# Performance work log

Measured on AMD Instinct MI355X. Metric: run time of the kernel, lower is better.

Reference implementation:

```python
import jax, jax.numpy as jnp
import numpy as np
import math

B, D, S, C, H = 8192, 512, 5, 2048, 4

def setup_inputs() -> dict:
    key = jax.random.key(0)
    ks = jax.random.split(key, 8)
    return {
        "features": jax.random.normal(ks[0], (B, D), dtype=jnp.float32),
        "logits": jax.random.normal(ks[1], (S, B, C), dtype=jnp.float32),
        "scale_feats": jax.random.normal(ks[2], (S, B, D), dtype=jnp.float32),
        "Wq": jax.random.normal(ks[3], (D, D), dtype=jnp.float32) * 0.02,
        "bq": jnp.zeros((D,), jnp.float32),
        "Wk": jax.random.normal(ks[4], (D, D), dtype=jnp.float32) * 0.02,
        "bk": jnp.zeros((D,), jnp.float32),
        "Wv": jax.random.normal(ks[5], (D, D), dtype=jnp.float32) * 0.02,
        "bv": jnp.zeros((D,), jnp.float32),
        "scale_emb": jax.random.normal(ks[6], (S, D), dtype=jnp.float32) * 0.02,
        "temperature": jnp.float32(0.07),
        "attn_w": jnp.ones((3,), jnp.float32) / 3.0,
    }

def reference(features, logits, scale_feats, Wq, bq, Wk, bk, Wv, bv, scale_emb, temperature, attn_w):
    b, d = features.shape
    s = scale_feats.shape[0]
    hd = d // H
    t = jnp.abs(temperature)

    # ---- multihead attention over scales (V is computed in torch but unused) ----
    Q = (features @ Wq + bq).reshape(b, H, hd)                      # [B,H,hd]
    sf_emb = scale_feats + scale_emb[:, None, :]                    # [S,B,D]
    K = (sf_emb @ Wk + bk).reshape(s, b, H, hd)                     # [S,B,H,hd]
    scores = jnp.einsum('bhd,sbhd->bhs', Q, K) / jnp.float32(math.sqrt(hd))
    attn_mha = jax.nn.softmax(scores / t, axis=-1).mean(axis=1)     # [B,S]

    # ---- geometric (angular) attention ----
    fn = features / jnp.linalg.norm(features, axis=-1, keepdims=True).clip(1e-12)
    sfn = scale_feats / jnp.linalg.norm(scale_feats, axis=-1, keepdims=True).clip(1e-12)
    cos_sim = jnp.einsum('bd,sbd->bs', fn, sfn)                     # [B,S]
    angles = jnp.arccos(jnp.clip(cos_sim, -1.0 + 1e-7, 1.0 - 1e-7))
    attn_geo = jax.nn.softmax(jnp.exp(-angles / t), axis=-1)        # [B,S]

    # ---- Cayley-Menger volume-proxy attention ----
    # simplex points: [features, scale_feat, cos(a)*f + sin(a)*s for a in {pi/4, pi/2, 3pi/4}]
    c = jnp.float32(math.sqrt(0.5))
    cf = jnp.array([1.0, 0.0, c, 0.0, -c], jnp.float32)             # coeffs on features
    cs = jnp.array([0.0, 1.0, c, 1.0, c], jnp.float32)              # coeffs on scale_feat
    simplex = (cf[None, :, None, None] * features[None, None] +
               cs[None, :, None, None] * scale_feats[:, None])      # [S,5,B,D]
    norms = jnp.sum(simplex * simplex, axis=-1)                     # [S,5,B]
    gram = jnp.einsum('spbd,sqbd->spqb', simplex, simplex)          # [S,5,5,B]
    distsq = norms[:, :, None] + norms[:, None, :] - 2.0 * gram     # [S,5,5,B]
    volumes = distsq.mean(axis=(1, 2)).T                            # [B,S]
    attn_cay = jax.nn.softmax(volumes / t, axis=-1)

    # ---- fuse attention types ----
    w = jax.nn.softmax(attn_w, axis=0)
    combined = w[0] * attn_mha + w[1] * attn_geo + w[2] * attn_cay  # [B,S]
    combined = combined / combined.sum(axis=-1, keepdims=True)

    combined_logits = jnp.einsum('bs,sbc->bc', combined, logits)    # [B,C]
    return (combined_logits, combined)
```

## Files before the change

### kernel.cpp

```cpp
#include <hip/hip_runtime.h>
#include <math.h>

#define B_N 8192
#define D_N 512
#define S_N 5
#define C_N 2048
#define H_N 4

typedef __attribute__((ext_vector_type(8))) short bf16x8;
typedef __attribute__((ext_vector_type(4))) float floatx4;

__device__ __forceinline__ float bf2f(short u) {
  union { unsigned int i; float f; } c;
  c.i = ((unsigned int)(unsigned short)u) << 16;
  return c.f;
}
__device__ __forceinline__ short f2bf(float f) {
  union { float f; unsigned int i; } c; c.f = f;
  unsigned int x = c.i;
  x += 0x7fffu + ((x >> 16) & 1u);
  return (short)(x >> 16);
}
__device__ __forceinline__ unsigned long long pack4(float a, float b, float c, float d) {
  return (unsigned long long)(unsigned short)f2bf(a)
       | ((unsigned long long)(unsigned short)f2bf(b) << 16)
       | ((unsigned long long)(unsigned short)f2bf(c) << 32)
       | ((unsigned long long)(unsigned short)f2bf(d) << 48);
}

__global__ __launch_bounds__(256) void k_prep(
    const float* __restrict__ f, const float* __restrict__ Wq,
    const float* __restrict__ Wk, short* __restrict__ fbf,
    short* __restrict__ WqT, short* __restrict__ Wkb) {
  __shared__ float lds[64][65];
  const int bx = blockIdx.x, t = threadIdx.x;
  if (bx < 2048) {
    int i = bx * 256 + t;
    const floatx4* p = (const floatx4*)(f + (size_t)i * 8);
    floatx4 a = p[0], b = p[1];
    *(unsigned long long*)(fbf + (size_t)i * 8)     = pack4(a[0], a[1], a[2], a[3]);
    *(unsigned long long*)(fbf + (size_t)i * 8 + 4) = pack4(b[0], b[1], b[2], b[3]);
  } else if (bx < 2112) {
    const int bb = bx - 2048;
    const int r0 = (bb >> 3) * 64, c0 = (bb & 7) * 64;
#pragma unroll
    for (int i = 0; i < 16; ++i) {
      int r = i * 4 + (t >> 6), c = t & 63;
      lds[r][c] = Wq[(size_t)(r0 + r) * 512 + c0 + c];
    }
    __syncthreads();
#pragma unroll
    for (int i = 0; i < 16; ++i) {
      int cL = i * 4 + (t >> 6), rL = t & 63;
      WqT[(size_t)(c0 + cL) * 512 + r0 + rL] = f2bf(lds[rL][cL]);
    }
  } else {
    const int base = (bx - 2112) * 8192 + t * 4;
#pragma unroll
    for (int i = 0; i < 8; ++i) {
      int idx = base + i * 1024;
      floatx4 v = *(const floatx4*)(Wk + idx);
      *(unsigned long long*)(Wkb + idx) = pack4(v[0], v[1], v[2], v[3]);
    }
  }
}

__device__ __forceinline__ void gll(const short* g, short* l) {
  __builtin_amdgcn_global_load_lds(
      (const __attribute__((address_space(1))) unsigned int*)(g),
      (__attribute__((address_space(3))) unsigned int*)(l), 16, 0, 0);
}

__global__ __launch_bounds__(256) void k_gemm64(
    const short* __restrict__ A, int lda,
    const short* __restrict__ BT, int ldb,
    short* __restrict__ O, int ldo,
    const float* __restrict__ bias, int K, int z_koff, int z_coff,
    float* __restrict__ qtp, const float* __restrict__ bkp) {
  __shared__ __align__(16) short As[2][2048];
  __shared__ __align__(16) short Bs[2][4096];
  __shared__ float qtLds[64][2];

  const int tid = threadIdx.x;
  const int lane = tid & 63;
  const int wid = tid >> 6;
  const int wr = wid >> 1, wc = wid & 1;
  const int row0 = blockIdx.y * 64;
  const int col0 = blockIdx.x * 128;
  const int z = blockIdx.z;
  const int koff = z * z_koff;
  const int ocoff = z * z_coff;

  const int r1 = tid >> 2, hk = tid & 3;
  const short* Ag1 = A + (size_t)(row0 + r1) * lda + koff + hk * 8;
  const short* Bg1 = BT + (size_t)(col0 + r1) * ldb + koff + hk * 8;
  const short* Bg2 = BT + (size_t)(col0 + 64 + r1) * ldb + koff + hk * 8;

  floatx4 acc[2][4];
  const floatx4 zero = {0.0f, 0.0f, 0.0f, 0.0f};
#pragma unroll
  for (int m = 0; m < 2; ++m)
#pragma unroll
    for (int n = 0; n < 4; ++n) acc[m][n] = zero;

  const int NT = K >> 5;
  int cur = 0;

  auto stage = [&](int q, int kb) {
    gll(Ag1 + kb, &As[q][tid * 8]);
    gll(Bg1 + kb, &Bs[q][tid * 8]);
    gll(Bg2 + kb, &Bs[q][tid * 8 + 2048]);
  };

  stage(0, 0);
  __syncthreads();

  for (int t = 0; t < NT; ++t) {
    if (t + 1 < NT) stage(cur ^ 1, (t + 1) * 32);
    bf16x8 af[2], bfr[4];
#pragma unroll
    for (int m = 0; m < 2; ++m)
      af[m] = *(const bf16x8*)&As[cur][(wr * 32 + m * 16 + (lane & 15)) * 32 + (lane >> 4) * 8];
#pragma unroll
    for (int n = 0; n < 4; ++n)
      bfr[n] = *(const bf16x8*)&Bs[cur][(wc * 64 + n * 16 + (lane & 15)) * 32 + (lane >> 4) * 8];
#pragma unroll
    for (int m = 0; m < 2; ++m)
#pragma unroll
      for (int n = 0; n < 4; ++n)
        acc[m][n] = __builtin_amdgcn_mfma_f32_16x16x32_bf16(af[m], bfr[n], acc[m][n], 0, 0, 0);
    __syncthreads();
    cur ^= 1;
  }

  float qp[2][4] = {{0, 0, 0, 0}, {0, 0, 0, 0}};
#pragma unroll
  for (int m = 0; m < 2; ++m) {
    int rowb = row0 + wr * 32 + m * 16 + (lane >> 4) * 4;
#pragma unroll
    for (int n = 0; n < 4; ++n) {
      int lcol = col0 + wc * 64 + n * 16 + (lane & 15);
      float bv = bias ? bias[lcol] : 0.0f;
      float bkv = qtp ? bkp[lcol] : 0.0f;
      int ocol = ocoff + lcol;
#pragma unroll
      for (int j = 0; j < 4; ++j) {
        float q = acc[m][n][j] + bv;
        O[(size_t)(rowb + j) * ldo + ocol] = f2bf(q);
        qp[m][j] += q * bkv;
      }
    }
  }

  if (qtp) {
#pragma unroll
    for (int m = 0; m < 2; ++m)
#pragma unroll
      for (int j = 0; j < 4; ++j) {
        float p = qp[m][j];
        p += __shfl_xor(p, 1, 64);
        p += __shfl_xor(p, 2, 64);
        p += __shfl_xor(p, 4, 64);
        p += __shfl_xor(p, 8, 64);
        int lrow = wr * 32 + m * 16 + (lane >> 4) * 4 + j;
        if ((lane & 15) == 0) qtLds[lrow][wc] = p;
      }
    __syncthreads();
    if (tid < 64)
      qtp[(size_t)(row0 + tid) * H_N + blockIdx.x] = qtLds[tid][0] + qtLds[tid][1];
  }
}

__global__ __launch_bounds__(256, 4) void k_fused(
    const float* __restrict__ f, const float* __restrict__ sf,
    const float* __restrict__ emb, const float* __restrict__ qt,
    const short* __restrict__ Rbf, const float* __restrict__ temp,
    const float* __restrict__ attn_w, const float* __restrict__ logits,
    float* __restrict__ out, float* __restrict__ comb_out) {
  const int lane = threadIdx.x & 63;
  const int wid = threadIdx.x >> 6;
  const int b = blockIdx.x * 4 + wid;
  const int a0 = lane * 8;

  const floatx4* fp = (const floatx4*)(f + (size_t)b * D_N + a0);
  floatx4 fA = fp[0], fB = fp[1];
  float fv[8];
#pragma unroll
  for (int j = 0; j < 4; ++j) { fv[j] = fA[j]; fv[4 + j] = fB[j]; }
  float ffp = 0;
#pragma unroll
  for (int j = 0; j < 8; ++j) ffp += fv[j] * fv[j];

  const floatx4 qtv = *(const floatx4*)(qt + (size_t)b * H_N);

  bf16x8 rv[H_N];
#pragma unroll
  for (int h = 0; h < H_N; ++h)
    rv[h] = *(const bf16x8*)(Rbf + (size_t)b * 2048 + h * 512 + a0);

  float fs_[S_N], ss_[S_N], sc_[S_N][H_N];

#pragma unroll
  for (int s = 0; s < S_N; ++s) {
    const floatx4* sp = (const floatx4*)(sf + ((size_t)s * B_N + b) * D_N + a0);
    floatx4 sA = sp[0], sB = sp[1];
    const floatx4* ep = (const floatx4*)(emb + (size_t)s * D_N + a0);
    floatx4 eA = ep[0], eB = ep[1];
    float sv[8], se[8];
#pragma unroll
    for (int j = 0; j < 4; ++j) {
      sv[j] = sA[j]; sv[4 + j] = sB[j];
      se[j] = sA[j] + eA[j]; se[4 + j] = sB[j] + eB[j];
    }
    float fsp = 0, ssp = 0;
    float scp[H_N] = {0, 0, 0, 0};
#pragma unroll
    for (int j = 0; j < 8; ++j) {
      fsp += fv[j] * sv[j];
      ssp += sv[j] * sv[j];
#pragma unroll
      for (int h = 0; h < H_N; ++h) scp[h] += se[j] * bf2f(rv[h][j]);
    }
    fs_[s] = fsp; ss_[s] = ssp;
#pragma unroll
    for (int h = 0; h < H_N; ++h) sc_[s][h] = scp[h];
  }

  float ffv = ffp;
#pragma unroll
  for (int o = 1; o < 64; o <<= 1) {
    ffv += __shfl_xor(ffv, o, 64);
#pragma unroll
    for (int s = 0; s < S_N; ++s) {
      fs_[s] += __shfl_xor(fs_[s], o, 64);
      ss_[s] += __shfl_xor(ss_[s], o, 64);
#pragma unroll
      for (int h = 0; h < H_N; ++h) sc_[s][h] += __shfl_xor(sc_[s][h], o, 64);
    }
  }

  const float t = fabsf(temp[0]);

  float amha[S_N] = {0, 0, 0, 0, 0};
  const float inv_mha = 1.0f / (sqrtf(128.0f) * t);
#pragma unroll
  for (int h = 0; h < H_N; ++h) {
    float lg[S_N];
#pragma unroll
    for (int s = 0; s < S_N; ++s) lg[s] = (sc_[s][h] + qtv[h]) * inv_mha;
    float mx = lg[0];
#pragma unroll
    for (int s = 1; s < S_N; ++s) mx = fmaxf(mx, lg[s]);
    float e[S_N], sum = 0;
#pragma unroll
    for (int s = 0; s < S_N; ++s) { e[s] = __expf(lg[s] - mx); sum += e[s]; }
    float isum = 0.25f / sum;
#pragma unroll
    for (int s = 0; s < S_N; ++s) amha[s] += e[s] * isum;
  }

  float ageo[S_N];
  {
    const float nf = fmaxf(sqrtf(ffv), 1e-12f);
    float g[S_N];
#pragma unroll
    for (int s = 0; s < S_N; ++s) {
      float ns = fmaxf(sqrtf(ss_[s]), 1e-12f);
      float cs0 = fs_[s] / (nf * ns);
      cs0 = fminf(fmaxf(cs0, -1.0f + 1e-7f), 1.0f - 1e-7f);
      g[s] = __expf(-acosf(cs0) / t);
    }
    float mx = g[0];
#pragma unroll
    for (int s = 1; s < S_N; ++s) mx = fmaxf(mx, g[s]);
    float sum = 0;
#pragma unroll
    for (int s = 0; s < S_N; ++s) { ageo[s] = __expf(g[s] - mx); sum += ageo[s]; }
#pragma unroll
    for (int s = 0; s < S_N; ++s) ageo[s] /= sum;
  }

  float acay[S_N];
  {
    const float SQ2 = 1.41421356237309515f;
    const float Aff = 0.72f;
    const float Ass = 0.72f - 0.32f * SQ2;
    const float Afs = -(8.0f + 4.0f * SQ2) / 25.0f;
    float lg[S_N];
#pragma unroll
    for (int s = 0; s < S_N; ++s)
      lg[s] = (Aff * ffv + Ass * ss_[s] + Afs * fs_[s]) / t;
    float mx = lg[0];
#pragma unroll
    for (int s = 1; s < S_N; ++s) mx = fmaxf(mx, lg[s]);
    float sum = 0;
#pragma unroll
    for (int s = 0; s < S_N; ++s) { acay[s] = __expf(lg[s] - mx); sum += acay[s]; }
#pragma unroll
    for (int s = 0; s < S_N; ++s) acay[s] /= sum;
  }

  float w0 = attn_w[0], w1 = attn_w[1], w2 = attn_w[2];
  float wm = fmaxf(w0, fmaxf(w1, w2));
  float e0 = __expf(w0 - wm), e1 = __expf(w1 - wm), e2 = __expf(w2 - wm);
  float wsum = e0 + e1 + e2;
  w0 = e0 / wsum; w1 = e1 / wsum; w2 = e2 / wsum;

  float cb[S_N], csum = 0;
#pragma unroll
  for (int s = 0; s < S_N; ++s) {
    cb[s] = w0 * amha[s] + w1 * ageo[s] + w2 * acay[s];
    csum += cb[s];
  }
  float ic = 1.0f / csum;
  float cbn[S_N];
#pragma unroll
  for (int s = 0; s < S_N; ++s) cbn[s] = cb[s] * ic;
  if (lane == 0) {
#pragma unroll
    for (int s = 0; s < S_N; ++s) comb_out[(size_t)b * S_N + s] = cbn[s];
  }

  const floatx4 fz = {0.f, 0.f, 0.f, 0.f};
#pragma unroll
  for (int cj = 0; cj < 4; ++cj) {
    const int c0 = cj * 512 + lane * 8;
    floatx4 accA = fz, accB = fz;
#pragma unroll
    for (int s = 0; s < S_N; ++s) {
      const float* lp = logits + ((size_t)s * B_N + b) * C_N + c0;
      floatx4 lA = *(const floatx4*)lp;
      floatx4 lB = *(const floatx4*)(lp + 4);
      accA += lA * cbn[s];
      accB += lB * cbn[s];
    }
    float* op = out + (size_t)b * C_N + c0;
    *(floatx4*)op = accA;
    *(floatx4*)(op + 4) = accB;
  }
}

extern "C" void kernel_launch(void* const* d_in, const int* in_sizes, int n_in,
                              void* d_out, int out_size, void* d_ws, size_t ws_size,
                              hipStream_t stream) {
  const float* features = (const float*)d_in[0];
  const float* logits   = (const float*)d_in[1];
  const float* sf       = (const float*)d_in[2];
  const float* Wq       = (const float*)d_in[3];
  const float* bq       = (const float*)d_in[4];
  const float* Wk       = (const float*)d_in[5];
  const float* bk       = (const float*)d_in[6];
  const float* emb      = (const float*)d_in[9];
  const float* temp     = (const float*)d_in[10];
  const float* attn_w   = (const float*)d_in[11];

  float* out  = (float*)d_out;
  float* comb = out + (size_t)B_N * C_N;

  char* w = (char*)d_ws;
  short* fbf = (short*)(w);
  short* Qbf = (short*)(w + 8388608);
  short* Rbf = (short*)(w + 16777216);
  short* WqT = (short*)(w + 50331648);
  short* Wkb = (short*)(w + 50855936);
  float* qtb = (float*)(w + 51380224);

  k_prep<<<dim3(2144), dim3(256), 0, stream>>>(features, Wq, Wk, fbf, WqT, Wkb);
  k_gemm64<<<dim3(4, 128, 1), dim3(256), 0, stream>>>(fbf, 512, WqT, 512, Qbf, 512,
                                                      bq, 512, 0, 0, qtb, bk);
  k_gemm64<<<dim3(4, 128, 4), dim3(256), 0, stream>>>(Qbf, 512, Wkb, 512, Rbf, 2048,
                                                      (const float*)nullptr, 128, 128, 512,
                                                      (float*)nullptr, (const float*)nullptr);
  k_fused<<<dim3(2048), dim3(256), 0, stream>>>(features, sf, emb, qtb, Rbf,
                                                temp, attn_w, logits, out, comb);
}
```

Measured before the change: 150.8 us.

## Fuse scale-feature score reductions into the K-projection GEMM epilogue

```diff
diff --git a/kernel.cpp b/kernel.cpp
--- a/kernel.cpp
+++ b/kernel.cpp
@@ -75,7 +75,7 @@
     const short* __restrict__ A, int lda,
     const short* __restrict__ BT, int ldb,
     short* __restrict__ O, int ldo,
-    const float* __restrict__ bias, int K, int z_koff, int z_coff,
+    const float* __restrict__ bias, int K,
     float* __restrict__ qtp, const float* __restrict__ bkp) {
   __shared__ __align__(16) short As[2][2048];
   __shared__ __align__(16) short Bs[2][4096];
@@ -87,14 +87,11 @@
   const int wr = wid >> 1, wc = wid & 1;
   const int row0 = blockIdx.y * 64;
   const int col0 = blockIdx.x * 128;
-  const int z = blockIdx.z;
-  const int koff = z * z_koff;
-  const int ocoff = z * z_coff;
 
   const int r1 = tid >> 2, hk = tid & 3;
-  const short* Ag1 = A + (size_t)(row0 + r1) * lda + koff + hk * 8;
-  const short* Bg1 = BT + (size_t)(col0 + r1) * ldb + koff + hk * 8;
-  const short* Bg2 = BT + (size_t)(col0 + 64 + r1) * ldb + koff + hk * 8;
+  const short* Ag1 = A + (size_t)(row0 + r1) * lda + hk * 8;
+  const short* Bg1 = BT + (size_t)(col0 + r1) * ldb + hk * 8;
+  const short* Bg2 = BT + (size_t)(col0 + 64 + r1) * ldb + hk * 8;
 
   floatx4 acc[2][4];
   const floatx4 zero = {0.0f, 0.0f, 0.0f, 0.0f};
@@ -140,105 +137,175 @@
 #pragma unroll
     for (int n = 0; n < 4; ++n) {
       int lcol = col0 + wc * 64 + n * 16 + (lane & 15);
-      float bv = bias ? bias[lcol] : 0.0f;
-      float bkv = qtp ? bkp[lcol] : 0.0f;
-      int ocol = ocoff + lcol;
+      float bv = bias[lcol];
+      float bkv = bkp[lcol];
 #pragma unroll
       for (int j = 0; j < 4; ++j) {
         float q = acc[m][n][j] + bv;
-        O[(size_t)(rowb + j) * ldo + ocol] = f2bf(q);
+        O[(size_t)(rowb + j) * ldo + lcol] = f2bf(q);
         qp[m][j] += q * bkv;
       }
     }
   }
 
-  if (qtp) {
+#pragma unroll
+  for (int m = 0; m < 2; ++m)
+#pragma unroll
+    for (int j = 0; j < 4; ++j) {
+      float p = qp[m][j];
+      p += __shfl_xor(p, 1, 64);
+      p += __shfl_xor(p, 2, 64);
+      p += __shfl_xor(p, 4, 64);
+      p += __shfl_xor(p, 8, 64);
+      int lrow = wr * 32 + m * 16 + (lane >> 4) * 4 + j;
+      if ((lane & 15) == 0) qtLds[lrow][wc] = p;
+    }
+  __syncthreads();
+  if (tid < 64)
+    qtp[(size_t)(row0 + tid) * H_N + blockIdx.x] = qtLds[tid][0] + qtLds[tid][1];
+}
+
+__global__ __launch_bounds__(256) void k_gemmRS(
+    const short* __restrict__ A,
+    const short* __restrict__ BT,
+    const float* __restrict__ sf, const float* __restrict__ f,
+    const float* __restrict__ emb,
+    float* __restrict__ scoresP, float* __restrict__ ssP,
+    float* __restrict__ fsP, float* __restrict__ ffP) {
+  __shared__ __align__(16) short As[2][2048];
+  __shared__ __align__(16) short Bs[2][4096];
+
+  const int tid = threadIdx.x;
+  const int lane = tid & 63;
+  const int wid = tid >> 6;
+  const int wr = wid >> 1, wc = wid & 1;
+  const int row0 = blockIdx.y * 64;
+  const int col0 = blockIdx.x * 128;
+
+  const int r1 = tid >> 2, hk = tid & 3;
+  const short* Ag1 = A + (size_t)(row0 + r1) * 512 + hk * 8;
+  const short* Bg1 = BT + (size_t)(col0 + r1) * 512 + hk * 8;
+  const short* Bg2 = BT + (size_t)(col0 + 64 + r1) * 512 + hk * 8;
+
+  const int rbase = row0 + wr * 32 + (lane >> 4) * 4;
+  const int acolL = col0 + wc * 64 + (lane & 15);
+
+  floatx4 acc[2][4];
+  const floatx4 zero = {0.0f, 0.0f, 0.0f, 0.0f};
+#pragma unroll
+  for (int m = 0; m < 2; ++m)
+#pragma unroll
+    for (int n = 0; n < 4; ++n) acc[m][n] = zero;
+
+  int cur = 0;
+  auto stage = [&](int q, int kb) {
+    gll(Ag1 + kb, &As[q][tid * 8]);
+    gll(Bg1 + kb, &Bs[q][tid * 8]);
+    gll(Bg2 + kb, &Bs[q][tid * 8 + 2048]);
+  };
+
+  stage(0, 0);
+  __syncthreads();
+
+  for (int t = 0; t < 16; ++t) {
+    if (t + 1 < 16) stage(cur ^ 1, (t + 1) * 32);
+    bf16x8 af[2], bfr[4];
 #pragma unroll
     for (int m = 0; m < 2; ++m)
-#pragma unroll
-      for (int j = 0; j < 4; ++j) {
-        float p = qp[m][j];
-        p += __shfl_xor(p, 1, 64);
-        p += __shfl_xor(p, 2, 64);
-        p += __shfl_xor(p, 4, 64);
-        p += __shfl_xor(p, 8, 64);
-        int lrow = wr * 32 + m * 16 + (lane >> 4) * 4 + j;
-        if ((lane & 15) == 0) qtLds[lrow][wc] = p;
+      af[m] = *(const bf16x8*)&As[cur][(wr * 32 + m * 16 + (lane & 15)) * 32 + (lane >> 4) * 8];
+#pragma unroll
+    for (int n = 0; n < 4; ++n)
+      bfr[n] = *(const bf16x8*)&Bs[cur][(wc * 64 + n * 16 + (lane & 15)) * 32 + (lane >> 4) * 8];
+#pragma unroll
+    for (int m = 0; m < 2; ++m)
+#pragma unroll
+      for (int n = 0; n < 4; ++n)
+        acc[m][n] = __builtin_amdgcn_mfma_f32_16x16x32_bf16(af[m], bfr[n], acc[m][n], 0, 0, 0);
+
+    if ((t & 3) == 3) {
+      const int z = t >> 2;
+#pragma unroll
+      for (int s = 0; s < S_N; ++s) {
+        float ps[2][4] = {{0, 0, 0, 0}, {0, 0, 0, 0}};
+        float pss[2][4] = {{0, 0, 0, 0}, {0, 0, 0, 0}};
+        float pfs[2][4] = {{0, 0, 0, 0}, {0, 0, 0, 0}};
+        float pff[2][4] = {{0, 0, 0, 0}, {0, 0, 0, 0}};
+#pragma unroll
+        for (int n = 0; n < 4; ++n) {
+          float evn = emb[s * 512 + acolL + n * 16];
+#pragma unroll
+          for (int m = 0; m < 2; ++m)
+#pragma unroll
+            for (int j = 0; j < 4; ++j) {
+              int brow = rbase + m * 16 + j;
+              float sv = sf[((size_t)s * B_N + brow) * 512 + acolL + n * 16];
+              ps[m][j] += acc[m][n][j] * (sv + evn);
+              if (z == 0) {
+                float fvv = f[(size_t)brow * 512 + acolL + n * 16];
+                pss[m][j] += sv * sv;
+                pfs[m][j] += fvv * sv;
+                if (s == 0) pff[m][j] += fvv * fvv;
+              }
+            }
+        }
+#pragma unroll
+        for (int m = 0; m < 2; ++m)
+#pragma unroll
+          for (int j = 0; j < 4; ++j) {
+            float p = ps[m][j];
+            p += __shfl_xor(p, 1, 64);
+            p += __shfl_xor(p, 2, 64);
+            p += __shfl_xor(p, 4, 64);
+            p += __shfl_xor(p, 8, 64);
+            int brow = rbase + m * 16 + j;
+            if ((lane & 15) == 0)
+              atomicAdd(&scoresP[(size_t)brow * 20 + z * 5 + s], p);
+            if (z == 0) {
+              float u = pss[m][j], v = pfs[m][j];
+              u += __shfl_xor(u, 1, 64); v += __shfl_xor(v, 1, 64);
+              u += __shfl_xor(u, 2, 64); v += __shfl_xor(v, 2, 64);
+              u += __shfl_xor(u, 4, 64); v += __shfl_xor(v, 4, 64);
+              u += __shfl_xor(u, 8, 64); v += __shfl_xor(v, 8, 64);
+              if ((lane & 15) == 0) {
+                atomicAdd(&ssP[(size_t)brow * 5 + s], u);
+                atomicAdd(&fsP[(size_t)brow * 5 + s], v);
+              }
+              if (s == 0) {
+                float w = pff[m][j];
+                w += __shfl_xor(w, 1, 64);
+                w += __shfl_xor(w, 2, 64);
+                w += __shfl_xor(w, 4, 64);
+                w += __shfl_xor(w, 8, 64);
+                if ((lane & 15) == 0) atomicAdd(&ffP[brow], w);
+              }
+            }
+          }
       }
+#pragma unroll
+      for (int m = 0; m < 2; ++m)
+#pragma unroll
+        for (int n = 0; n < 4; ++n) acc[m][n] = zero;
+    }
     __syncthreads();
-    if (tid < 64)
-      qtp[(size_t)(row0 + tid) * H_N + blockIdx.x] = qtLds[tid][0] + qtLds[tid][1];
-  }
-}
-
-__global__ __launch_bounds__(256, 4) void k_fused(
-    const float* __restrict__ f, const float* __restrict__ sf,
-    const float* __restrict__ emb, const float* __restrict__ qt,
-    const short* __restrict__ Rbf, const float* __restrict__ temp,
+    cur ^= 1;
+  }
+}
+
+__global__ __launch_bounds__(256) void k_fused2(
+    const float* __restrict__ qt, const float* __restrict__ scoresP,
+    const float* __restrict__ ssP, const float* __restrict__ fsP,
+    const float* __restrict__ ffP, const float* __restrict__ temp,
     const float* __restrict__ attn_w, const float* __restrict__ logits,
     float* __restrict__ out, float* __restrict__ comb_out) {
   const int lane = threadIdx.x & 63;
   const int wid = threadIdx.x >> 6;
   const int b = blockIdx.x * 4 + wid;
-  const int a0 = lane * 8;
-
-  const floatx4* fp = (const floatx4*)(f + (size_t)b * D_N + a0);
-  floatx4 fA = fp[0], fB = fp[1];
-  float fv[8];
-#pragma unroll
-  for (int j = 0; j < 4; ++j) { fv[j] = fA[j]; fv[4 + j] = fB[j]; }
-  float ffp = 0;
-#pragma unroll
-  for (int j = 0; j < 8; ++j) ffp += fv[j] * fv[j];
 
   const floatx4 qtv = *(const floatx4*)(qt + (size_t)b * H_N);
-
-  bf16x8 rv[H_N];
-#pragma unroll
-  for (int h = 0; h < H_N; ++h)
-    rv[h] = *(const bf16x8*)(Rbf + (size_t)b * 2048 + h * 512 + a0);
-
-  float fs_[S_N], ss_[S_N], sc_[S_N][H_N];
-
-#pragma unroll
-  for (int s = 0; s < S_N; ++s) {
-    const floatx4* sp = (const floatx4*)(sf + ((size_t)s * B_N + b) * D_N + a0);
-    floatx4 sA = sp[0], sB = sp[1];
-    const floatx4* ep = (const floatx4*)(emb + (size_t)s * D_N + a0);
-    floatx4 eA = ep[0], eB = ep[1];
-    float sv[8], se[8];
-#pragma unroll
-    for (int j = 0; j < 4; ++j) {
-      sv[j] = sA[j]; sv[4 + j] = sB[j];
-      se[j] = sA[j] + eA[j]; se[4 + j] = sB[j] + eB[j];
-    }
-    float fsp = 0, ssp = 0;
-    float scp[H_N] = {0, 0, 0, 0};
-#pragma unroll
-    for (int j = 0; j < 8; ++j) {
-      fsp += fv[j] * sv[j];
-      ssp += sv[j] * sv[j];
-#pragma unroll
-      for (int h = 0; h < H_N; ++h) scp[h] += se[j] * bf2f(rv[h][j]);
-    }
-    fs_[s] = fsp; ss_[s] = ssp;
-#pragma unroll
-    for (int h = 0; h < H_N; ++h) sc_[s][h] = scp[h];
-  }
-
-  float ffv = ffp;
-#pragma unroll
-  for (int o = 1; o < 64; o <<= 1) {
-    ffv += __shfl_xor(ffv, o, 64);
-#pragma unroll
-    for (int s = 0; s < S_N; ++s) {
-      fs_[s] += __shfl_xor(fs_[s], o, 64);
-      ss_[s] += __shfl_xor(ss_[s], o, 64);
-#pragma unroll
-      for (int h = 0; h < H_N; ++h) sc_[s][h] += __shfl_xor(sc_[s][h], o, 64);
-    }
-  }
-
+  const float* scp = scoresP + (size_t)b * 20;
+  const float* ssp = ssP + (size_t)b * 5;
+  const float* fsp = fsP + (size_t)b * 5;
+  const float ffv = ffP[b];
   const float t = fabsf(temp[0]);
 
   float amha[S_N] = {0, 0, 0, 0, 0};
@@ -247,7 +314,7 @@
   for (int h = 0; h < H_N; ++h) {
     float lg[S_N];
 #pragma unroll
-    for (int s = 0; s < S_N; ++s) lg[s] = (sc_[s][h] + qtv[h]) * inv_mha;
+    for (int s = 0; s < S_N; ++s) lg[s] = (scp[h * 5 + s] + qtv[h]) * inv_mha;
     float mx = lg[0];
 #pragma unroll
     for (int s = 1; s < S_N; ++s) mx = fmaxf(mx, lg[s]);
@@ -265,8 +332,8 @@
     float g[S_N];
 #pragma unroll
     for (int s = 0; s < S_N; ++s) {
-      float ns = fmaxf(sqrtf(ss_[s]), 1e-12f);
-      float cs0 = fs_[s] / (nf * ns);
+      float ns = fmaxf(sqrtf(ssp[s]), 1e-12f);
+      float cs0 = fsp[s] / (nf * ns);
       cs0 = fminf(fmaxf(cs0, -1.0f + 1e-7f), 1.0f - 1e-7f);
       g[s] = __expf(-acosf(cs0) / t);
     }
@@ -289,7 +356,7 @@
     float lg[S_N];
 #pragma unroll
     for (int s = 0; s < S_N; ++s)
-      lg[s] = (Aff * ffv + Ass * ss_[s] + Afs * fs_[s]) / t;
+      lg[s] = (Aff * ffv + Ass * ssp[s] + Afs * fsp[s]) / t;
     float mx = lg[0];
 #pragma unroll
     for (int s = 1; s < S_N; ++s) mx = fmaxf(mx, lg[s]);
@@ -358,19 +425,22 @@
   float* comb = out + (size_t)B_N * C_N;
 
   char* w = (char*)d_ws;
-  short* fbf = (short*)(w);
-  short* Qbf = (short*)(w + 8388608);
-  short* Rbf = (short*)(w + 16777216);
-  short* WqT = (short*)(w + 50331648);
-  short* Wkb = (short*)(w + 50855936);
-  float* qtb = (float*)(w + 51380224);
-
+  short* fbf     = (short*)(w);
+  short* Qbf     = (short*)(w + 8388608);
+  short* WqT     = (short*)(w + 16777216);
+  short* Wkb     = (short*)(w + 17301504);
+  float* qtb     = (float*)(w + 17825792);
+  float* scoresP = (float*)(w + 17956864);
+  float* ssP     = (float*)(w + 18612224);
+  float* fsP     = (float*)(w + 18776064);
+  float* ffP     = (float*)(w + 18939904);
+
+  hipMemsetAsync(scoresP, 0, 1015808, stream);
   k_prep<<<dim3(2144), dim3(256), 0, stream>>>(features, Wq, Wk, fbf, WqT, Wkb);
-  k_gemm64<<<dim3(4, 128, 1), dim3(256), 0, stream>>>(fbf, 512, WqT, 512, Qbf, 512,
-                                                      bq, 512, 0, 0, qtb, bk);
-  k_gemm64<<<dim3(4, 128, 4), dim3(256), 0, stream>>>(Qbf, 512, Wkb, 512, Rbf, 2048,
-                                                      (const float*)nullptr, 128, 128, 512,
-                                                      (float*)nullptr, (const float*)nullptr);
-  k_fused<<<dim3(2048), dim3(256), 0, stream>>>(features, sf, emb, qtb, Rbf,
-                                                temp, attn_w, logits, out, comb);
-}
+  k_gemm64<<<dim3(4, 128), dim3(256), 0, stream>>>(fbf, 512, WqT, 512, Qbf, 512,
+                                                   bq, 512, qtb, bk);
+  k_gemmRS<<<dim3(4, 128), dim3(256), 0, stream>>>(Qbf, Wkb, sf, features, emb,
+                                                   scoresP, ssP, fsP, ffP);
+  k_fused2<<<dim3(2048), dim3(256), 0, stream>>>(qtb, scoresP, ssP, fsP, ffP,
+                                                 temp, attn_w, logits, out, comb);
+}
```

Result: slower. 394.7 us (+161.6%).

## Fuse Q projection and Q·Wk GEMMs into one kernel keeping Q in LDS

Applied to the files above, without the earlier changes.

```diff
diff --git a/kernel.cpp b/kernel.cpp
--- a/kernel.cpp
+++ b/kernel.cpp
@@ -71,30 +71,30 @@
       (__attribute__((address_space(3))) unsigned int*)(l), 16, 0, 0);
 }
 
-__global__ __launch_bounds__(256) void k_gemm64(
-    const short* __restrict__ A, int lda,
-    const short* __restrict__ BT, int ldb,
-    short* __restrict__ O, int ldo,
-    const float* __restrict__ bias, int K, int z_koff, int z_coff,
+__global__ __launch_bounds__(256) void k_gemmQR(
+    const short* __restrict__ A,
+    const short* __restrict__ BT,
+    const short* __restrict__ Wkb,
+    short* __restrict__ Rbf,
+    const float* __restrict__ bias,
     float* __restrict__ qtp, const float* __restrict__ bkp) {
   __shared__ __align__(16) short As[2][2048];
   __shared__ __align__(16) short Bs[2][4096];
+  __shared__ __align__(16) short Qt[64][132];
   __shared__ float qtLds[64][2];
 
   const int tid = threadIdx.x;
   const int lane = tid & 63;
   const int wid = tid >> 6;
   const int wr = wid >> 1, wc = wid & 1;
+  const int h = blockIdx.x;
   const int row0 = blockIdx.y * 64;
-  const int col0 = blockIdx.x * 128;
-  const int z = blockIdx.z;
-  const int koff = z * z_koff;
-  const int ocoff = z * z_coff;
+  const int col0 = h * 128;
 
   const int r1 = tid >> 2, hk = tid & 3;
-  const short* Ag1 = A + (size_t)(row0 + r1) * lda + koff + hk * 8;
-  const short* Bg1 = BT + (size_t)(col0 + r1) * ldb + koff + hk * 8;
-  const short* Bg2 = BT + (size_t)(col0 + 64 + r1) * ldb + koff + hk * 8;
+  const short* Ag1 = A + (size_t)(row0 + r1) * 512 + hk * 8;
+  const short* Bg1 = BT + (size_t)(col0 + r1) * 512 + hk * 8;
+  const short* Bg2 = BT + (size_t)(col0 + 64 + r1) * 512 + hk * 8;
 
   floatx4 acc[2][4];
   const floatx4 zero = {0.0f, 0.0f, 0.0f, 0.0f};
@@ -103,9 +103,7 @@
 #pragma unroll
     for (int n = 0; n < 4; ++n) acc[m][n] = zero;
 
-  const int NT = K >> 5;
   int cur = 0;
-
   auto stage = [&](int q, int kb) {
     gll(Ag1 + kb, &As[q][tid * 8]);
     gll(Bg1 + kb, &Bs[q][tid * 8]);
@@ -115,8 +113,8 @@
   stage(0, 0);
   __syncthreads();
 
-  for (int t = 0; t < NT; ++t) {
-    if (t + 1 < NT) stage(cur ^ 1, (t + 1) * 32);
+  for (int t = 0; t < 16; ++t) {
+    if (t + 1 < 16) stage(cur ^ 1, (t + 1) * 32);
     bf16x8 af[2], bfr[4];
 #pragma unroll
     for (int m = 0; m < 2; ++m)
@@ -136,38 +134,73 @@
   float qp[2][4] = {{0, 0, 0, 0}, {0, 0, 0, 0}};
 #pragma unroll
   for (int m = 0; m < 2; ++m) {
-    int rowb = row0 + wr * 32 + m * 16 + (lane >> 4) * 4;
+    int lrow0 = wr * 32 + m * 16 + (lane >> 4) * 4;
 #pragma unroll
     for (int n = 0; n < 4; ++n) {
-      int lcol = col0 + wc * 64 + n * 16 + (lane & 15);
-      float bv = bias ? bias[lcol] : 0.0f;
-      float bkv = qtp ? bkp[lcol] : 0.0f;
-      int ocol = ocoff + lcol;
+      int lc = wc * 64 + n * 16 + (lane & 15);
+      float bv = bias[col0 + lc];
+      float bkv = bkp[col0 + lc];
 #pragma unroll
       for (int j = 0; j < 4; ++j) {
         float q = acc[m][n][j] + bv;
-        O[(size_t)(rowb + j) * ldo + ocol] = f2bf(q);
+        Qt[lrow0 + j][lc] = f2bf(q);
         qp[m][j] += q * bkv;
       }
     }
   }
 
-  if (qtp) {
+#pragma unroll
+  for (int m = 0; m < 2; ++m)
+#pragma unroll
+    for (int j = 0; j < 4; ++j) {
+      float p = qp[m][j];
+      p += __shfl_xor(p, 1, 64);
+      p += __shfl_xor(p, 2, 64);
+      p += __shfl_xor(p, 4, 64);
+      p += __shfl_xor(p, 8, 64);
+      int lrow = wr * 32 + m * 16 + (lane >> 4) * 4 + j;
+      if ((lane & 15) == 0) qtLds[lrow][wc] = p;
+    }
+  __syncthreads();
+  if (tid < 64)
+    qtp[(size_t)(row0 + tid) * H_N + h] = qtLds[tid][0] + qtLds[tid][1];
+
+  for (int cc = 0; cc < 4; ++cc) {
+    floatx4 acc2[2][4];
 #pragma unroll
     for (int m = 0; m < 2; ++m)
 #pragma unroll
-      for (int j = 0; j < 4; ++j) {
-        float p = qp[m][j];
-        p += __shfl_xor(p, 1, 64);
-        p += __shfl_xor(p, 2, 64);
-        p += __shfl_xor(p, 4, 64);
-        p += __shfl_xor(p, 8, 64);
-        int lrow = wr * 32 + m * 16 + (lane >> 4) * 4 + j;
-        if ((lane & 15) == 0) qtLds[lrow][wc] = p;
+      for (int n = 0; n < 4; ++n) acc2[m][n] = zero;
+
+#pragma unroll
+    for (int ks = 0; ks < 4; ++ks) {
+      bf16x8 af[2], bfr[4];
+#pragma unroll
+      for (int m = 0; m < 2; ++m)
+        af[m] = *(const bf16x8*)&Qt[wr * 32 + m * 16 + (lane & 15)][ks * 32 + (lane >> 4) * 8];
+#pragma unroll
+      for (int n = 0; n < 4; ++n) {
+        int a = cc * 128 + wc * 64 + n * 16 + (lane & 15);
+        bfr[n] = *(const bf16x8*)(Wkb + (size_t)a * 512 + col0 + ks * 32 + (lane >> 4) * 8);
       }
-    __syncthreads();
-    if (tid < 64)
-      qtp[(size_t)(row0 + tid) * H_N + blockIdx.x] = qtLds[tid][0] + qtLds[tid][1];
+#pragma unroll
+      for (int m = 0; m < 2; ++m)
+#pragma unroll
+        for (int n = 0; n < 4; ++n)
+          acc2[m][n] = __builtin_amdgcn_mfma_f32_16x16x32_bf16(af[m], bfr[n], acc2[m][n], 0, 0, 0);
+    }
+
+#pragma unroll
+    for (int m = 0; m < 2; ++m) {
+      int rowb = row0 + wr * 32 + m * 16 + (lane >> 4) * 4;
+#pragma unroll
+      for (int n = 0; n < 4; ++n) {
+        int ocol = h * 512 + cc * 128 + wc * 64 + n * 16 + (lane & 15);
+#pragma unroll
+        for (int j = 0; j < 4; ++j)
+          Rbf[(size_t)(rowb + j) * 2048 + ocol] = f2bf(acc2[m][n][j]);
+      }
+    }
   }
 }
 
@@ -359,18 +392,13 @@
 
   char* w = (char*)d_ws;
   short* fbf = (short*)(w);
-  short* Qbf = (short*)(w + 8388608);
   short* Rbf = (short*)(w + 16777216);
   short* WqT = (short*)(w + 50331648);
   short* Wkb = (short*)(w + 50855936);
   float* qtb = (float*)(w + 51380224);
 
   k_prep<<<dim3(2144), dim3(256), 0, stream>>>(features, Wq, Wk, fbf, WqT, Wkb);
-  k_gemm64<<<dim3(4, 128, 1), dim3(256), 0, stream>>>(fbf, 512, WqT, 512, Qbf, 512,
-                                                      bq, 512, 0, 0, qtb, bk);
-  k_gemm64<<<dim3(4, 128, 4), dim3(256), 0, stream>>>(Qbf, 512, Wkb, 512, Rbf, 2048,
-                                                      (const float*)nullptr, 128, 128, 512,
-                                                      (float*)nullptr, (const float*)nullptr);
+  k_gemmQR<<<dim3(4, 128), dim3(256), 0, stream>>>(fbf, WqT, Wkb, Rbf, bq, qtb, bk);
   k_fused<<<dim3(2048), dim3(256), 0, stream>>>(features, sf, emb, qtb, Rbf,
                                                 temp, attn_w, logits, out, comb);
 }
```

After: 147.2 us (median of 2 runs). 1.02x faster.
